# Kernel optimization log

Hardware: AMD Instinct MI355X
Metric: run time of the kernel (lower is better)

## Reference

```python
import jax, jax.numpy as jnp
import numpy as np

BATCH, SEQ_LEN, NOISE_DIM, SEQ_DIM, HID = 8192, 256, 8, 4, 64

def setup_inputs() -> dict:
    key = jax.random.key(0)
    ks = jax.random.split(key, 6)
    s = lambda k, shp, fan: jax.random.normal(k, shp, jnp.float32) * (1.0 / np.sqrt(fan))
    return {
        "noise": jax.random.normal(ks[0], (BATCH, SEQ_LEN, NOISE_DIM), jnp.float32),
        "Wx": s(ks[1], (SEQ_DIM + NOISE_DIM, 4 * HID), SEQ_DIM + NOISE_DIM),
        "Wh": s(ks[2], (HID, 4 * HID), HID),
        "b": jnp.zeros((4 * HID,), jnp.float32),
        "W1": s(ks[3], (HID, HID), HID), "b1": jnp.zeros((HID,), jnp.float32),
        "W2": s(ks[4], (HID, HID), HID), "b2": jnp.zeros((HID,), jnp.float32),
        "W3": s(ks[5], (HID, SEQ_DIM), HID), "b3": jnp.zeros((SEQ_DIM,), jnp.float32),
    }

def reference(noise, Wx, Wh, b, W1, b1, W2, b2, W3, b3):
    batch = noise.shape[0]
    # log_series=True -> initial x is zeros
    x0 = jnp.zeros((batch, SEQ_DIM), noise.dtype)
    h0 = jnp.zeros((batch, HID), noise.dtype)
    c0 = jnp.zeros((batch, HID), noise.dtype)
    noise_t = jnp.swapaxes(noise[:, : SEQ_LEN - 1, :], 0, 1)  # [L-1, B, noise_dim]

    def step(carry, n_t):
        x, h, c = carry
        inp = jnp.concatenate([x, n_t], axis=-1)           # [B, seq_dim+noise_dim]
        z = inp @ Wx + h @ Wh + b                          # [B, 4H], keras gate order i,f,g,o
        i, f, g, o = jnp.split(z, 4, axis=-1)
        c = jax.nn.sigmoid(f) * c + jax.nn.sigmoid(i) * jnp.tanh(g)
        h = jax.nn.sigmoid(o) * jnp.tanh(c)
        y = jax.nn.relu(h @ W1 + b1)
        y = jax.nn.relu(y @ W2 + b2)
        x_new = y @ W3 + b3                                # [B, seq_dim]
        return (x_new, h, c), x_new

    _, xs = jax.lax.scan(step, (x0, h0, c0), noise_t)       # [L-1, B, seq_dim]
    seq = jnp.concatenate([x0[None], xs], axis=0)           # [L, B, seq_dim]
    seq = jnp.swapaxes(seq, 0, 1)                           # [B, L, seq_dim]
    return jnp.cumsum(seq, axis=1)
```

## Files before the change

### kernel.cpp

```cpp
#include <hip/hip_runtime.h>


typedef _Float16 h8 __attribute__((ext_vector_type(8)));
typedef __fp16 p2h __attribute__((ext_vector_type(2)));
typedef float f4 __attribute__((ext_vector_type(4)));

#define MFMA(a, b, c) __builtin_amdgcn_mfma_f32_16x16x32_f16(a, b, c, 0, 0, 0)
#define EXP2(x) __builtin_amdgcn_exp2f(x)

constexpr int SEQ = 256, STEPS = 255, ND = 8, SD = 4, HID = 64, G4 = 256;
constexpr int HST = 72;
constexpr float LOG2E = 1.44269504f;

__device__ __forceinline__ void store4h(_Float16* p, f4 v) {
    p2h lo = __builtin_amdgcn_cvt_pkrtz(v[0], v[1]);
    p2h hi = __builtin_amdgcn_cvt_pkrtz(v[2], v[3]);
    float2 st;
    st.x = __builtin_bit_cast(float, lo);
    st.y = __builtin_bit_cast(float, hi);
    *(float2*)p = st;
}

__global__ __launch_bounds__(256, 2) void genlstm_kernel(
    const float* __restrict__ noise, const float* __restrict__ Wx,
    const float* __restrict__ Wh, const float* __restrict__ b,
    const float* __restrict__ W1, const float* __restrict__ b1,
    const float* __restrict__ W2, const float* __restrict__ b2,
    const float* __restrict__ W3, const float* __restrict__ b3,
    float* __restrict__ out)
{
    __shared__ alignas(16) _Float16 Hb[16 * HST];
    __shared__ alignas(16) _Float16 Y1b[16 * HST];
    __shared__ alignas(16) _Float16 Y2b[16 * HST];

    const int tid = threadIdx.x, wid = tid >> 6, lane = tid & 63;
    const int col = lane & 15, quad = lane >> 4, q8 = quad * 8;
    const int row0 = blockIdx.x * 16;
    const int n0 = wid * 16 + col;
    const int wq = wid * 16 + quad * 4;

    const float gsc[4] = {LOG2E, LOG2E, 2.f * LOG2E, LOG2E};

    h8 wg[4][2];
    #pragma unroll
    for (int g = 0; g < 4; ++g)
        #pragma unroll
        for (int s = 0; s < 2; ++s)
            #pragma unroll
            for (int j = 0; j < 8; ++j)
                wg[g][s][j] = (_Float16)(Wh[(32 * s + q8 + j) * G4 + 64 * g + n0] * gsc[g]);

    h8 wgn[4];
    #pragma unroll
    for (int g = 0; g < 4; ++g)
        #pragma unroll
        for (int j = 0; j < 8; ++j) {
            const int k = q8 + j;
            const int n = 64 * g + n0;
            float v = 0.0f;
            if (k < 8) v = Wx[(4 + k) * G4 + n];
            else if (k == 8) {
                float bx = b3[0] * Wx[0 * G4 + n] + b3[1] * Wx[1 * G4 + n] +
                           b3[2] * Wx[2 * G4 + n] + b3[3] * Wx[3 * G4 + n];
                v = b[n] + bx;
            }
            wgn[g][j] = (_Float16)(v * gsc[g]);
        }

    h8 wgy[4][2];
    #pragma unroll
    for (int s = 0; s < 2; ++s)
        #pragma unroll
        for (int j = 0; j < 8; ++j) {
            const int k = 32 * s + q8 + j;
            const float w30 = W3[k * SD + 0], w31 = W3[k * SD + 1];
            const float w32 = W3[k * SD + 2], w33 = W3[k * SD + 3];
            #pragma unroll
            for (int g = 0; g < 4; ++g) {
                const int n = 64 * g + n0;
                float acc = w30 * Wx[0 * G4 + n] + w31 * Wx[1 * G4 + n] +
                            w32 * Wx[2 * G4 + n] + w33 * Wx[3 * G4 + n];
                wgy[g][s][j] = (_Float16)(acc * gsc[g]);
            }
        }
    h8 w1f[2], w2f[2], w3f[2];
    #pragma unroll
    for (int s = 0; s < 2; ++s)
        #pragma unroll
        for (int j = 0; j < 8; ++j) {
            const int k = 32 * s + q8 + j;
            w1f[s][j] = (_Float16)W1[k * HID + n0];
            w2f[s][j] = (_Float16)W2[k * HID + n0];
            w3f[s][j] = (_Float16)(col < 4 ? W3[k * SD + col] : 0.0f);
        }
    f4 b1v, b2v, b3v;
    #pragma unroll
    for (int r = 0; r < 4; ++r) {
        b1v[r] = b1[wq + r];
        b2v[r] = b2[wq + r];
        b3v[r] = (quad == 0) ? b3[r] : 0.0f;
    }

    if (tid < 16) {
        float4 z; z.x = z.y = z.z = z.w = 0.0f;
        *(float4*)(out + (size_t)(row0 + tid) * SEQ * SD) = z;
    }

    _Float16* Hrow = &Hb[col * HST];
    _Float16* Y1row = &Y1b[col * HST];
    _Float16* Y2row = &Y2b[col * HST];
    float* outp = out + ((size_t)(row0 + col) * SEQ + 1) * SD;

    const float* npt = noise + (size_t)(row0 + col) * SEQ * ND;

    const f4 fz = {0.f, 0.f, 0.f, 0.f};
    f4 cst = fz, run = fz;
    f4 zi, zf, zg, zo;

    float4 nf0, nf1;
    nf0.x = nf0.y = nf0.z = nf0.w = 0.f;
    nf1 = nf0;

    if (blockIdx.x & 256) __builtin_amdgcn_s_sleep(26);

    {
        if (quad == 0) { nf0 = *(const float4*)npt; nf1 = *(const float4*)(npt + 4); }
        npt += ND;
        union { h8 v; p2h p[4]; } nb;
        nb.p[0] = __builtin_amdgcn_cvt_pkrtz(nf0.x, nf0.y);
        nb.p[1] = __builtin_amdgcn_cvt_pkrtz(nf0.z, nf0.w);
        nb.p[2] = __builtin_amdgcn_cvt_pkrtz(nf1.x, nf1.y);
        nb.p[3] = __builtin_amdgcn_cvt_pkrtz(nf1.z, nf1.w);
        #pragma unroll
        for (int g = 0; g < 4; ++g) {
            f4 tb;
            #pragma unroll
            for (int r = 0; r < 4; ++r) tb[r] = b[64 * g + wq + r] * gsc[g];
            f4 z0 = MFMA(wgn[g], nb.v, tb);
            if (g == 0) zi = z0; else if (g == 1) zf = z0;
            else if (g == 2) zg = z0; else zo = z0;
        }
        if (quad == 1) nf0.x = 1.0f;
    }

    #pragma unroll 1
    for (int t = 0; t < STEPS; ++t) {
        if (quad == 0) { nf0 = *(const float4*)npt; nf1 = *(const float4*)(npt + 4); }
        npt += ND;

        f4 hv;
        #pragma unroll
        for (int r = 0; r < 4; ++r) {
            float Ei = EXP2(-fmaxf(zi[r], -15.f * LOG2E));
            float Ef = EXP2(-fmaxf(zf[r], -15.f * LOG2E));
            float Eg = EXP2(-fmaxf(zg[r], -30.f * LOG2E));
            float Eo = EXP2(-zo[r]);
            float Di = 1.f + Ei, Df = 1.f + Ef, Dg = 1.f + Eg, Do = 1.f + Eo;
            float DiDg = Di * Dg;
            float cn = (cst[r] * DiDg + (2.f - Dg) * Df) *
                       __builtin_amdgcn_rcpf(Df * DiDg);
            cst[r] = cn;
            float Ec = EXP2(fmaxf(cn, -15.f) * (-2.f * LOG2E));
            hv[r] = (1.f - Ec) * __builtin_amdgcn_rcpf(Do * (1.f + Ec));
        }
        store4h(Hrow + wq, hv);
        __syncthreads();

        __builtin_amdgcn_s_setprio(1);

        h8 h0 = *(const h8*)(&Hb[col * HST] + q8);
        h8 h1 = *(const h8*)(&Hb[col * HST] + 32 + q8);

        f4 y1 = MFMA(w1f[0], h0, b1v);
        y1 = MFMA(w1f[1], h1, y1);
        #pragma unroll
        for (int r = 0; r < 4; ++r) y1[r] = fmaxf(y1[r], 0.f);
        store4h(Y1row + wq, y1);

        zi = MFMA(wg[0][0], h0, fz); zi = MFMA(wg[0][1], h1, zi);
        zf = MFMA(wg[1][0], h0, fz); zf = MFMA(wg[1][1], h1, zf);
        zg = MFMA(wg[2][0], h0, fz); zg = MFMA(wg[2][1], h1, zg);
        zo = MFMA(wg[3][0], h0, fz); zo = MFMA(wg[3][1], h1, zo);
        __syncthreads();

        h8 p0 = *(const h8*)(Y1row + q8);
        h8 p1 = *(const h8*)(Y1row + 32 + q8);
        f4 y2 = MFMA(w2f[0], p0, b2v);
        y2 = MFMA(w2f[1], p1, y2);
        #pragma unroll
        for (int r = 0; r < 4; ++r) y2[r] = fmaxf(y2[r], 0.f);
        store4h(Y2row + wq, y2);
        __syncthreads();

        h8 q0 = *(const h8*)(Y2row + q8);
        h8 q1 = *(const h8*)(Y2row + 32 + q8);

        zi = MFMA(wgy[0][0], q0, zi); zi = MFMA(wgy[0][1], q1, zi);
        zf = MFMA(wgy[1][0], q0, zf); zf = MFMA(wgy[1][1], q1, zf);
        zg = MFMA(wgy[2][0], q0, zg); zg = MFMA(wgy[2][1], q1, zg);
        zo = MFMA(wgy[3][0], q0, zo); zo = MFMA(wgy[3][1], q1, zo);

        union { h8 v; p2h p[4]; } nb;
        nb.p[0] = __builtin_amdgcn_cvt_pkrtz(nf0.x, nf0.y);
        nb.p[1] = __builtin_amdgcn_cvt_pkrtz(nf0.z, nf0.w);
        nb.p[2] = __builtin_amdgcn_cvt_pkrtz(nf1.x, nf1.y);
        nb.p[3] = __builtin_amdgcn_cvt_pkrtz(nf1.z, nf1.w);
        zi = MFMA(wgn[0], nb.v, zi);
        zf = MFMA(wgn[1], nb.v, zf);
        zg = MFMA(wgn[2], nb.v, zg);
        zo = MFMA(wgn[3], nb.v, zo);

        if (wid == 0) {
            f4 x = MFMA(w3f[0], q0, b3v);
            x = MFMA(w3f[1], q1, x);
            if (quad == 0) {
                run += x;
                *(f4*)outp = run;
            }
        }
        outp += SD;

        __builtin_amdgcn_s_setprio(0);
    }
}

extern "C" void kernel_launch(void* const* d_in, const int* in_sizes, int n_in,
                              void* d_out, int out_size, void* d_ws, size_t ws_size,
                              hipStream_t stream) {
    genlstm_kernel<<<512, 256, 0, stream>>>(
        (const float*)d_in[0], (const float*)d_in[1], (const float*)d_in[2],
        (const float*)d_in[3], (const float*)d_in[4], (const float*)d_in[5],
        (const float*)d_in[6], (const float*)d_in[7], (const float*)d_in[8],
        (const float*)d_in[9], (float*)d_out);
}
```

Baseline: 364.4 us.

## Pair two independent row groups per block with phase-staggered LSTM pipeline

Each block now carries two 16-row groups of four waves each, in 512-thread blocks with half as many blocks. The two groups run the three phases of a step (gate nonlinearity plus output, the Y1 MLP layer, the Y2 layer) offset by one phase, so they share the same barriers. While one group does elementwise and transcendental work, the other issues MFMAs, which is meant to hide the serial dependency chain and barrier latency. The sleep-based stagger is removed. The cost is that each barrier now covers eight waves, and the grid has half as many blocks.

Measured after the change: 623.0 us. 71.0% more time.

```diff
diff --git a/kernel.cpp b/kernel.cpp
--- a/kernel.cpp
+++ b/kernel.cpp
@@ -21,7 +21,7 @@
     *(float2*)p = st;
 }
 
-__global__ __launch_bounds__(256, 2) void genlstm_kernel(
+__global__ __launch_bounds__(512, 2) void genlstm_kernel(
     const float* __restrict__ noise, const float* __restrict__ Wx,
     const float* __restrict__ Wh, const float* __restrict__ b,
     const float* __restrict__ W1, const float* __restrict__ b1,
@@ -29,15 +29,18 @@
     const float* __restrict__ W3, const float* __restrict__ b3,
     float* __restrict__ out)
 {
-    __shared__ alignas(16) _Float16 Hb[16 * HST];
-    __shared__ alignas(16) _Float16 Y1b[16 * HST];
-    __shared__ alignas(16) _Float16 Y2b[16 * HST];
+    __shared__ alignas(16) _Float16 Hb[2][16 * HST];
+    __shared__ alignas(16) _Float16 Y1b[2][16 * HST];
+    __shared__ alignas(16) _Float16 Y2b[2][16 * HST];
 
     const int tid = threadIdx.x, wid = tid >> 6, lane = tid & 63;
+    const int grp = wid >> 2;
+    const int wv = wid & 3;
     const int col = lane & 15, quad = lane >> 4, q8 = quad * 8;
-    const int row0 = blockIdx.x * 16;
-    const int n0 = wid * 16 + col;
-    const int wq = wid * 16 + quad * 4;
+    const int brow = blockIdx.x * 32;
+    const int row0 = brow + grp * 16;
+    const int n0 = wv * 16 + col;
+    const int wq = wv * 16 + quad * 4;
 
     const float gsc[4] = {LOG2E, LOG2E, 2.f * LOG2E, LOG2E};
 
@@ -101,14 +104,14 @@
         b3v[r] = (quad == 0) ? b3[r] : 0.0f;
     }
 
-    if (tid < 16) {
+    if (tid < 32) {
         float4 z; z.x = z.y = z.z = z.w = 0.0f;
-        *(float4*)(out + (size_t)(row0 + tid) * SEQ * SD) = z;
-    }
-
-    _Float16* Hrow = &Hb[col * HST];
-    _Float16* Y1row = &Y1b[col * HST];
-    _Float16* Y2row = &Y2b[col * HST];
+        *(float4*)(out + (size_t)(brow + tid) * SEQ * SD) = z;
+    }
+
+    _Float16* Hrow = &Hb[grp][col * HST];
+    _Float16* Y1row = &Y1b[grp][col * HST];
+    _Float16* Y2row = &Y2b[grp][col * HST];
     float* outp = out + ((size_t)(row0 + col) * SEQ + 1) * SD;
 
     const float* npt = noise + (size_t)(row0 + col) * SEQ * ND;
@@ -120,8 +123,6 @@
     float4 nf0, nf1;
     nf0.x = nf0.y = nf0.z = nf0.w = 0.f;
     nf1 = nf0;
-
-    if (blockIdx.x & 256) __builtin_amdgcn_s_sleep(26);
 
     {
         if (quad == 0) { nf0 = *(const float4*)npt; nf1 = *(const float4*)(npt + 4); }
@@ -143,46 +144,76 @@
         if (quad == 1) nf0.x = 1.0f;
     }
 
-    #pragma unroll 1
-    for (int t = 0; t < STEPS; ++t) {
-        if (quad == 0) { nf0 = *(const float4*)npt; nf1 = *(const float4*)(npt + 4); }
-        npt += ND;
-
-        f4 hv;
-        #pragma unroll
-        for (int r = 0; r < 4; ++r) {
-            float Ei = EXP2(-fmaxf(zi[r], -15.f * LOG2E));
-            float Ef = EXP2(-fmaxf(zf[r], -15.f * LOG2E));
-            float Eg = EXP2(-fmaxf(zg[r], -30.f * LOG2E));
-            float Eo = EXP2(-zo[r]);
-            float Di = 1.f + Ei, Df = 1.f + Ef, Dg = 1.f + Eg, Do = 1.f + Eo;
-            float DiDg = Di * Dg;
-            float cn = (cst[r] * DiDg + (2.f - Dg) * Df) *
-                       __builtin_amdgcn_rcpf(Df * DiDg);
-            cst[r] = cn;
-            float Ec = EXP2(fmaxf(cn, -15.f) * (-2.f * LOG2E));
-            hv[r] = (1.f - Ec) * __builtin_amdgcn_rcpf(Do * (1.f + Ec));
-        }
-        store4h(Hrow + wq, hv);
-        __syncthreads();
-
+    auto segC = [&](int t) {
+        if (t > 0) {
+            h8 q0 = *(const h8*)(Y2row + q8);
+            h8 q1 = *(const h8*)(Y2row + 32 + q8);
+            union { h8 v; p2h p[4]; } nb;
+            nb.p[0] = __builtin_amdgcn_cvt_pkrtz(nf0.x, nf0.y);
+            nb.p[1] = __builtin_amdgcn_cvt_pkrtz(nf0.z, nf0.w);
+            nb.p[2] = __builtin_amdgcn_cvt_pkrtz(nf1.x, nf1.y);
+            nb.p[3] = __builtin_amdgcn_cvt_pkrtz(nf1.z, nf1.w);
+            if (t < STEPS && quad == 0) {
+                nf0 = *(const float4*)npt; nf1 = *(const float4*)(npt + 4);
+            }
+            npt += ND;
+            zi = MFMA(wgn[0], nb.v, zi);
+            zf = MFMA(wgn[1], nb.v, zf);
+            zg = MFMA(wgn[2], nb.v, zg);
+            zo = MFMA(wgn[3], nb.v, zo);
+            zi = MFMA(wgy[0][0], q0, zi); zi = MFMA(wgy[0][1], q1, zi);
+            zf = MFMA(wgy[1][0], q0, zf); zf = MFMA(wgy[1][1], q1, zf);
+            zg = MFMA(wgy[2][0], q0, zg); zg = MFMA(wgy[2][1], q1, zg);
+            zo = MFMA(wgy[3][0], q0, zo); zo = MFMA(wgy[3][1], q1, zo);
+            if (wv == 0) {
+                f4 x = MFMA(w3f[0], q0, b3v);
+                x = MFMA(w3f[1], q1, x);
+                if (quad == 0) {
+                    run += x;
+                    *(f4*)outp = run;
+                }
+            }
+            outp += SD;
+        } else {
+            if (quad == 0) { nf0 = *(const float4*)npt; nf1 = *(const float4*)(npt + 4); }
+            npt += ND;
+        }
+        if (t < STEPS) {
+            f4 hv;
+            #pragma unroll
+            for (int r = 0; r < 4; ++r) {
+                float Ei = EXP2(-fmaxf(zi[r], -15.f * LOG2E));
+                float Ef = EXP2(-fmaxf(zf[r], -15.f * LOG2E));
+                float Eg = EXP2(-fmaxf(zg[r], -30.f * LOG2E));
+                float Eo = EXP2(-zo[r]);
+                float Di = 1.f + Ei, Df = 1.f + Ef, Dg = 1.f + Eg, Do = 1.f + Eo;
+                float DiDg = Di * Dg;
+                float cn = (cst[r] * DiDg + (2.f - Dg) * Df) *
+                           __builtin_amdgcn_rcpf(Df * DiDg);
+                cst[r] = cn;
+                float Ec = EXP2(fmaxf(cn, -15.f) * (-2.f * LOG2E));
+                hv[r] = (1.f - Ec) * __builtin_amdgcn_rcpf(Do * (1.f + Ec));
+            }
+            store4h(Hrow + wq, hv);
+        }
+    };
+    auto segY1 = [&]() {
         __builtin_amdgcn_s_setprio(1);
-
-        h8 h0 = *(const h8*)(&Hb[col * HST] + q8);
-        h8 h1 = *(const h8*)(&Hb[col * HST] + 32 + q8);
-
+        h8 h0 = *(const h8*)(Hrow + q8);
+        h8 h1 = *(const h8*)(Hrow + 32 + q8);
         f4 y1 = MFMA(w1f[0], h0, b1v);
         y1 = MFMA(w1f[1], h1, y1);
         #pragma unroll
         for (int r = 0; r < 4; ++r) y1[r] = fmaxf(y1[r], 0.f);
         store4h(Y1row + wq, y1);
-
         zi = MFMA(wg[0][0], h0, fz); zi = MFMA(wg[0][1], h1, zi);
         zf = MFMA(wg[1][0], h0, fz); zf = MFMA(wg[1][1], h1, zf);
         zg = MFMA(wg[2][0], h0, fz); zg = MFMA(wg[2][1], h1, zg);
         zo = MFMA(wg[3][0], h0, fz); zo = MFMA(wg[3][1], h1, zo);
-        __syncthreads();
-
+        __builtin_amdgcn_s_setprio(0);
+    };
+    auto segY2 = [&]() {
+        __builtin_amdgcn_s_setprio(1);
         h8 p0 = *(const h8*)(Y1row + q8);
         h8 p1 = *(const h8*)(Y1row + 32 + q8);
         f4 y2 = MFMA(w2f[0], p0, b2v);
@@ -190,44 +221,28 @@
         #pragma unroll
         for (int r = 0; r < 4; ++r) y2[r] = fmaxf(y2[r], 0.f);
         store4h(Y2row + wq, y2);
+        __builtin_amdgcn_s_setprio(0);
+    };
+
+    if (grp) segC(0);
+    __syncthreads();
+
+    #pragma unroll 1
+    for (int t = 0; t < STEPS; ++t) {
+        if (!grp) segC(t);   else segY1();
         __syncthreads();
-
-        h8 q0 = *(const h8*)(Y2row + q8);
-        h8 q1 = *(const h8*)(Y2row + 32 + q8);
-
-        zi = MFMA(wgy[0][0], q0, zi); zi = MFMA(wgy[0][1], q1, zi);
-        zf = MFMA(wgy[1][0], q0, zf); zf = MFMA(wgy[1][1], q1, zf);
-        zg = MFMA(wgy[2][0], q0, zg); zg = MFMA(wgy[2][1], q1, zg);
-        zo = MFMA(wgy[3][0], q0, zo); zo = MFMA(wgy[3][1], q1, zo);
-
-        union { h8 v; p2h p[4]; } nb;
-        nb.p[0] = __builtin_amdgcn_cvt_pkrtz(nf0.x, nf0.y);
-        nb.p[1] = __builtin_amdgcn_cvt_pkrtz(nf0.z, nf0.w);
-        nb.p[2] = __builtin_amdgcn_cvt_pkrtz(nf1.x, nf1.y);
-        nb.p[3] = __builtin_amdgcn_cvt_pkrtz(nf1.z, nf1.w);
-        zi = MFMA(wgn[0], nb.v, zi);
-        zf = MFMA(wgn[1], nb.v, zf);
-        zg = MFMA(wgn[2], nb.v, zg);
-        zo = MFMA(wgn[3], nb.v, zo);
-
-        if (wid == 0) {
-            f4 x = MFMA(w3f[0], q0, b3v);
-            x = MFMA(w3f[1], q1, x);
-            if (quad == 0) {
-                run += x;
-                *(f4*)outp = run;
-            }
-        }
-        outp += SD;
-
-        __builtin_amdgcn_s_setprio(0);
-    }
+        if (!grp) segY1();   else segY2();
+        __syncthreads();
+        if (!grp) segY2();   else segC(t + 1);
+        __syncthreads();
+    }
+    if (!grp) segC(STEPS);
 }
 
 extern "C" void kernel_launch(void* const* d_in, const int* in_sizes, int n_in,
                               void* d_out, int out_size, void* d_ws, size_t ws_size,
                               hipStream_t stream) {
-    genlstm_kernel<<<512, 256, 0, stream>>>(
+    genlstm_kernel<<<256, 512, 0, stream>>>(
         (const float*)d_in[0], (const float*)d_in[1], (const float*)d_in[2],
         (const float*)d_in[3], (const float*)d_in[4], (const float*)d_in[5],
         (const float*)d_in[6], (const float*)d_in[7], (const float*)d_in[8],
```

## Split LSTM gate and MLP head work into specialized warp groups

Applied to the files above, without the earlier changes.

Adds two extra wavefronts per block (384 threads) that handle the MLP head (W1, W2, W3 and the output cumsum). The original four waves now compute only the LSTM gates. Barrier counts are matched across both roles: the gate waves issue a double syncthreads while the MLP waves do their two layers. The aim is to take the MLP MFMAs and their register-held weights off the gate waves and ease register pressure, at the cost of more threads per block and the same serial barrier chain.

Result: slower. 608.3 us (+66.9%).

```diff
diff --git a/kernel.cpp b/kernel.cpp
--- a/kernel.cpp
+++ b/kernel.cpp
@@ -21,7 +21,7 @@
     *(float2*)p = st;
 }
 
-__global__ __launch_bounds__(256, 2) void genlstm_kernel(
+__global__ __launch_bounds__(384, 2) void genlstm_kernel(
     const float* __restrict__ noise, const float* __restrict__ Wx,
     const float* __restrict__ Wh, const float* __restrict__ b,
     const float* __restrict__ W1, const float* __restrict__ b1,
@@ -36,198 +36,232 @@
     const int tid = threadIdx.x, wid = tid >> 6, lane = tid & 63;
     const int col = lane & 15, quad = lane >> 4, q8 = quad * 8;
     const int row0 = blockIdx.x * 16;
-    const int n0 = wid * 16 + col;
-    const int wq = wid * 16 + quad * 4;
-
-    const float gsc[4] = {LOG2E, LOG2E, 2.f * LOG2E, LOG2E};
-
-    h8 wg[4][2];
-    #pragma unroll
-    for (int g = 0; g < 4; ++g)
-        #pragma unroll
-        for (int s = 0; s < 2; ++s)
-            #pragma unroll
-            for (int j = 0; j < 8; ++j)
-                wg[g][s][j] = (_Float16)(Wh[(32 * s + q8 + j) * G4 + 64 * g + n0] * gsc[g]);
-
-    h8 wgn[4];
-    #pragma unroll
-    for (int g = 0; g < 4; ++g)
-        #pragma unroll
-        for (int j = 0; j < 8; ++j) {
-            const int k = q8 + j;
-            const int n = 64 * g + n0;
-            float v = 0.0f;
-            if (k < 8) v = Wx[(4 + k) * G4 + n];
-            else if (k == 8) {
-                float bx = b3[0] * Wx[0 * G4 + n] + b3[1] * Wx[1 * G4 + n] +
-                           b3[2] * Wx[2 * G4 + n] + b3[3] * Wx[3 * G4 + n];
-                v = b[n] + bx;
-            }
-            wgn[g][j] = (_Float16)(v * gsc[g]);
-        }
-
-    h8 wgy[4][2];
-    #pragma unroll
-    for (int s = 0; s < 2; ++s)
-        #pragma unroll
-        for (int j = 0; j < 8; ++j) {
-            const int k = 32 * s + q8 + j;
-            const float w30 = W3[k * SD + 0], w31 = W3[k * SD + 1];
-            const float w32 = W3[k * SD + 2], w33 = W3[k * SD + 3];
-            #pragma unroll
-            for (int g = 0; g < 4; ++g) {
-                const int n = 64 * g + n0;
-                float acc = w30 * Wx[0 * G4 + n] + w31 * Wx[1 * G4 + n] +
-                            w32 * Wx[2 * G4 + n] + w33 * Wx[3 * G4 + n];
-                wgy[g][s][j] = (_Float16)(acc * gsc[g]);
-            }
-        }
-    h8 w1f[2], w2f[2], w3f[2];
-    #pragma unroll
-    for (int s = 0; s < 2; ++s)
-        #pragma unroll
-        for (int j = 0; j < 8; ++j) {
-            const int k = 32 * s + q8 + j;
-            w1f[s][j] = (_Float16)W1[k * HID + n0];
-            w2f[s][j] = (_Float16)W2[k * HID + n0];
-            w3f[s][j] = (_Float16)(col < 4 ? W3[k * SD + col] : 0.0f);
-        }
-    f4 b1v, b2v, b3v;
-    #pragma unroll
-    for (int r = 0; r < 4; ++r) {
-        b1v[r] = b1[wq + r];
-        b2v[r] = b2[wq + r];
-        b3v[r] = (quad == 0) ? b3[r] : 0.0f;
-    }
 
     if (tid < 16) {
         float4 z; z.x = z.y = z.z = z.w = 0.0f;
         *(float4*)(out + (size_t)(row0 + tid) * SEQ * SD) = z;
     }
 
-    _Float16* Hrow = &Hb[col * HST];
-    _Float16* Y1row = &Y1b[col * HST];
-    _Float16* Y2row = &Y2b[col * HST];
-    float* outp = out + ((size_t)(row0 + col) * SEQ + 1) * SD;
-
-    const float* npt = noise + (size_t)(row0 + col) * SEQ * ND;
-
-    const f4 fz = {0.f, 0.f, 0.f, 0.f};
-    f4 cst = fz, run = fz;
-    f4 zi, zf, zg, zo;
-
-    float4 nf0, nf1;
-    nf0.x = nf0.y = nf0.z = nf0.w = 0.f;
-    nf1 = nf0;
-
     if (blockIdx.x & 256) __builtin_amdgcn_s_sleep(26);
 
-    {
-        if (quad == 0) { nf0 = *(const float4*)npt; nf1 = *(const float4*)(npt + 4); }
-        npt += ND;
-        union { h8 v; p2h p[4]; } nb;
-        nb.p[0] = __builtin_amdgcn_cvt_pkrtz(nf0.x, nf0.y);
-        nb.p[1] = __builtin_amdgcn_cvt_pkrtz(nf0.z, nf0.w);
-        nb.p[2] = __builtin_amdgcn_cvt_pkrtz(nf1.x, nf1.y);
-        nb.p[3] = __builtin_amdgcn_cvt_pkrtz(nf1.z, nf1.w);
-        #pragma unroll
-        for (int g = 0; g < 4; ++g) {
-            f4 tb;
-            #pragma unroll
-            for (int r = 0; r < 4; ++r) tb[r] = b[64 * g + wq + r] * gsc[g];
-            f4 z0 = MFMA(wgn[g], nb.v, tb);
-            if (g == 0) zi = z0; else if (g == 1) zf = z0;
-            else if (g == 2) zg = z0; else zo = z0;
-        }
-        if (quad == 1) nf0.x = 1.0f;
-    }
-
-    #pragma unroll 1
-    for (int t = 0; t < STEPS; ++t) {
-        if (quad == 0) { nf0 = *(const float4*)npt; nf1 = *(const float4*)(npt + 4); }
-        npt += ND;
-
-        f4 hv;
+    if (wid < 4) {
+        const int wv = wid;
+        const int n0 = wv * 16 + col;
+        const int wq = wv * 16 + quad * 4;
+        const float gsc[4] = {LOG2E, LOG2E, 2.f * LOG2E, LOG2E};
+
+        h8 wg[4][2];
+        #pragma unroll
+        for (int g = 0; g < 4; ++g)
+            #pragma unroll
+            for (int s = 0; s < 2; ++s)
+                #pragma unroll
+                for (int j = 0; j < 8; ++j)
+                    wg[g][s][j] = (_Float16)(Wh[(32 * s + q8 + j) * G4 + 64 * g + n0] * gsc[g]);
+
+        h8 wgn[4];
+        #pragma unroll
+        for (int g = 0; g < 4; ++g)
+            #pragma unroll
+            for (int j = 0; j < 8; ++j) {
+                const int k = q8 + j;
+                const int n = 64 * g + n0;
+                float v = 0.0f;
+                if (k < 8) v = Wx[(4 + k) * G4 + n];
+                else if (k == 8) {
+                    float bx = b3[0] * Wx[0 * G4 + n] + b3[1] * Wx[1 * G4 + n] +
+                               b3[2] * Wx[2 * G4 + n] + b3[3] * Wx[3 * G4 + n];
+                    v = b[n] + bx;
+                }
+                wgn[g][j] = (_Float16)(v * gsc[g]);
+            }
+
+        h8 wgy[4][2];
+        #pragma unroll
+        for (int s = 0; s < 2; ++s)
+            #pragma unroll
+            for (int j = 0; j < 8; ++j) {
+                const int k = 32 * s + q8 + j;
+                const float w30 = W3[k * SD + 0], w31 = W3[k * SD + 1];
+                const float w32 = W3[k * SD + 2], w33 = W3[k * SD + 3];
+                #pragma unroll
+                for (int g = 0; g < 4; ++g) {
+                    const int n = 64 * g + n0;
+                    float acc = w30 * Wx[0 * G4 + n] + w31 * Wx[1 * G4 + n] +
+                                w32 * Wx[2 * G4 + n] + w33 * Wx[3 * G4 + n];
+                    wgy[g][s][j] = (_Float16)(acc * gsc[g]);
+                }
+            }
+
+        _Float16* Hrow = &Hb[col * HST];
+        const _Float16* Y2row = &Y2b[col * HST];
+        const float* npt = noise + (size_t)(row0 + col) * SEQ * ND;
+
+        const f4 fz = {0.f, 0.f, 0.f, 0.f};
+        f4 cst = fz;
+        f4 zi, zf, zg, zo;
+        float4 nf0, nf1;
+        nf0.x = nf0.y = nf0.z = nf0.w = 0.f;
+        nf1 = nf0;
+
+        {
+            if (quad == 0) { nf0 = *(const float4*)npt; nf1 = *(const float4*)(npt + 4); }
+            npt += ND;
+            union { h8 v; p2h p[4]; } nb;
+            nb.p[0] = __builtin_amdgcn_cvt_pkrtz(nf0.x, nf0.y);
+            nb.p[1] = __builtin_amdgcn_cvt_pkrtz(nf0.z, nf0.w);
+            nb.p[2] = __builtin_amdgcn_cvt_pkrtz(nf1.x, nf1.y);
+            nb.p[3] = __builtin_amdgcn_cvt_pkrtz(nf1.z, nf1.w);
+            #pragma unroll
+            for (int g = 0; g < 4; ++g) {
+                f4 tb;
+                #pragma unroll
+                for (int r = 0; r < 4; ++r) tb[r] = b[64 * g + wq + r] * gsc[g];
+                f4 z0 = MFMA(wgn[g], nb.v, tb);
+                if (g == 0) zi = z0; else if (g == 1) zf = z0;
+                else if (g == 2) zg = z0; else zo = z0;
+            }
+            if (quad == 1) nf0.x = 1.0f;
+        }
+
+        __builtin_amdgcn_s_setprio(1);
+        #pragma unroll 1
+        for (int t = 0; t < STEPS; ++t) {
+            if (quad == 0) { nf0 = *(const float4*)npt; nf1 = *(const float4*)(npt + 4); }
+            npt += ND;
+
+            f4 hv;
+            #pragma unroll
+            for (int r = 0; r < 4; ++r) {
+                float Ei = EXP2(-fmaxf(zi[r], -15.f * LOG2E));
+                float Ef = EXP2(-fmaxf(zf[r], -15.f * LOG2E));
+                float Eg = EXP2(-fmaxf(zg[r], -30.f * LOG2E));
+                float Eo = EXP2(-zo[r]);
+                float Di = 1.f + Ei, Df = 1.f + Ef, Dg = 1.f + Eg, Do = 1.f + Eo;
+                float DiDg = Di * Dg;
+                float cn = (cst[r] * DiDg + (2.f - Dg) * Df) *
+                           __builtin_amdgcn_rcpf(Df * DiDg);
+                cst[r] = cn;
+                float Ec = EXP2(fmaxf(cn, -15.f) * (-2.f * LOG2E));
+                hv[r] = (1.f - Ec) * __builtin_amdgcn_rcpf(Do * (1.f + Ec));
+            }
+            store4h(Hrow + wq, hv);
+            __syncthreads();
+            __builtin_amdgcn_s_setprio(0);
+
+            zi = MFMA(wg[0][0], *(const h8*)(Hrow + q8), fz);
+            zi = MFMA(wg[0][1], *(const h8*)(Hrow + 32 + q8), zi);
+            {
+                h8 h0 = *(const h8*)(Hrow + q8);
+                h8 h1 = *(const h8*)(Hrow + 32 + q8);
+                zf = MFMA(wg[1][0], h0, fz); zf = MFMA(wg[1][1], h1, zf);
+                zg = MFMA(wg[2][0], h0, fz); zg = MFMA(wg[2][1], h1, zg);
+                zo = MFMA(wg[3][0], h0, fz); zo = MFMA(wg[3][1], h1, zo);
+            }
+            __syncthreads();
+            __syncthreads();
+            __builtin_amdgcn_s_setprio(1);
+
+            h8 q0 = *(const h8*)(Y2row + q8);
+            h8 q1 = *(const h8*)(Y2row + 32 + q8);
+            union { h8 v; p2h p[4]; } nb;
+            nb.p[0] = __builtin_amdgcn_cvt_pkrtz(nf0.x, nf0.y);
+            nb.p[1] = __builtin_amdgcn_cvt_pkrtz(nf0.z, nf0.w);
+            nb.p[2] = __builtin_amdgcn_cvt_pkrtz(nf1.x, nf1.y);
+            nb.p[3] = __builtin_amdgcn_cvt_pkrtz(nf1.z, nf1.w);
+            zi = MFMA(wgn[0], nb.v, zi);
+            zf = MFMA(wgn[1], nb.v, zf);
+            zg = MFMA(wgn[2], nb.v, zg);
+            zo = MFMA(wgn[3], nb.v, zo);
+            zi = MFMA(wgy[0][0], q0, zi); zi = MFMA(wgy[0][1], q1, zi);
+            zf = MFMA(wgy[1][0], q0, zf); zf = MFMA(wgy[1][1], q1, zf);
+            zg = MFMA(wgy[2][0], q0, zg); zg = MFMA(wgy[2][1], q1, zg);
+            zo = MFMA(wgy[3][0], q0, zo); zo = MFMA(wgy[3][1], q1, zo);
+        }
+    } else {
+        const int mw = wid - 4;
+        h8 w1m[2][2], w2m[2][2], w3f[2];
+        #pragma unroll
+        for (int tn = 0; tn < 2; ++tn)
+            #pragma unroll
+            for (int s = 0; s < 2; ++s)
+                #pragma unroll
+                for (int j = 0; j < 8; ++j) {
+                    const int k = 32 * s + q8 + j;
+                    const int n = 32 * mw + 16 * tn + col;
+                    w1m[tn][s][j] = (_Float16)W1[k * HID + n];
+                    w2m[tn][s][j] = (_Float16)W2[k * HID + n];
+                }
+        #pragma unroll
+        for (int s = 0; s < 2; ++s)
+            #pragma unroll
+            for (int j = 0; j < 8; ++j) {
+                const int k = 32 * s + q8 + j;
+                w3f[s][j] = (_Float16)((mw == 0 && col < 4) ? W3[k * SD + col] : 0.0f);
+            }
+        f4 b1m[2], b2m[2], b3v;
         #pragma unroll
         for (int r = 0; r < 4; ++r) {
-            float Ei = EXP2(-fmaxf(zi[r], -15.f * LOG2E));
-            float Ef = EXP2(-fmaxf(zf[r], -15.f * LOG2E));
-            float Eg = EXP2(-fmaxf(zg[r], -30.f * LOG2E));
-            float Eo = EXP2(-zo[r]);
-            float Di = 1.f + Ei, Df = 1.f + Ef, Dg = 1.f + Eg, Do = 1.f + Eo;
-            float DiDg = Di * Dg;
-            float cn = (cst[r] * DiDg + (2.f - Dg) * Df) *
-                       __builtin_amdgcn_rcpf(Df * DiDg);
-            cst[r] = cn;
-            float Ec = EXP2(fmaxf(cn, -15.f) * (-2.f * LOG2E));
-            hv[r] = (1.f - Ec) * __builtin_amdgcn_rcpf(Do * (1.f + Ec));
-        }
-        store4h(Hrow + wq, hv);
-        __syncthreads();
+            #pragma unroll
+            for (int tn = 0; tn < 2; ++tn) {
+                b1m[tn][r] = b1[32 * mw + 16 * tn + quad * 4 + r];
+                b2m[tn][r] = b2[32 * mw + 16 * tn + quad * 4 + r];
+            }
+            b3v[r] = (quad == 0) ? b3[r] : 0.0f;
+        }
+
+        const _Float16* Hrow = &Hb[col * HST];
+        _Float16* Y1row = &Y1b[col * HST];
+        _Float16* Y2row = &Y2b[col * HST];
+        float* outp = out + ((size_t)(row0 + col) * SEQ + 1) * SD;
+        const f4 fz = {0.f, 0.f, 0.f, 0.f};
+        f4 run = fz;
 
         __builtin_amdgcn_s_setprio(1);
-
-        h8 h0 = *(const h8*)(&Hb[col * HST] + q8);
-        h8 h1 = *(const h8*)(&Hb[col * HST] + 32 + q8);
-
-        f4 y1 = MFMA(w1f[0], h0, b1v);
-        y1 = MFMA(w1f[1], h1, y1);
-        #pragma unroll
-        for (int r = 0; r < 4; ++r) y1[r] = fmaxf(y1[r], 0.f);
-        store4h(Y1row + wq, y1);
-
-        zi = MFMA(wg[0][0], h0, fz); zi = MFMA(wg[0][1], h1, zi);
-        zf = MFMA(wg[1][0], h0, fz); zf = MFMA(wg[1][1], h1, zf);
-        zg = MFMA(wg[2][0], h0, fz); zg = MFMA(wg[2][1], h1, zg);
-        zo = MFMA(wg[3][0], h0, fz); zo = MFMA(wg[3][1], h1, zo);
-        __syncthreads();
-
-        h8 p0 = *(const h8*)(Y1row + q8);
-        h8 p1 = *(const h8*)(Y1row + 32 + q8);
-        f4 y2 = MFMA(w2f[0], p0, b2v);
-        y2 = MFMA(w2f[1], p1, y2);
-        #pragma unroll
-        for (int r = 0; r < 4; ++r) y2[r] = fmaxf(y2[r], 0.f);
-        store4h(Y2row + wq, y2);
-        __syncthreads();
-
-        h8 q0 = *(const h8*)(Y2row + q8);
-        h8 q1 = *(const h8*)(Y2row + 32 + q8);
-
-        zi = MFMA(wgy[0][0], q0, zi); zi = MFMA(wgy[0][1], q1, zi);
-        zf = MFMA(wgy[1][0], q0, zf); zf = MFMA(wgy[1][1], q1, zf);
-        zg = MFMA(wgy[2][0], q0, zg); zg = MFMA(wgy[2][1], q1, zg);
-        zo = MFMA(wgy[3][0], q0, zo); zo = MFMA(wgy[3][1], q1, zo);
-
-        union { h8 v; p2h p[4]; } nb;
-        nb.p[0] = __builtin_amdgcn_cvt_pkrtz(nf0.x, nf0.y);
-        nb.p[1] = __builtin_amdgcn_cvt_pkrtz(nf0.z, nf0.w);
-        nb.p[2] = __builtin_amdgcn_cvt_pkrtz(nf1.x, nf1.y);
-        nb.p[3] = __builtin_amdgcn_cvt_pkrtz(nf1.z, nf1.w);
-        zi = MFMA(wgn[0], nb.v, zi);
-        zf = MFMA(wgn[1], nb.v, zf);
-        zg = MFMA(wgn[2], nb.v, zg);
-        zo = MFMA(wgn[3], nb.v, zo);
-
-        if (wid == 0) {
-            f4 x = MFMA(w3f[0], q0, b3v);
-            x = MFMA(w3f[1], q1, x);
-            if (quad == 0) {
-                run += x;
-                *(f4*)outp = run;
-            }
-        }
-        outp += SD;
-
-        __builtin_amdgcn_s_setprio(0);
+        #pragma unroll 1
+        for (int t = 0; t < STEPS; ++t) {
+            __syncthreads();
+            h8 h0 = *(const h8*)(Hrow + q8);
+            h8 h1 = *(const h8*)(Hrow + 32 + q8);
+            #pragma unroll
+            for (int tn = 0; tn < 2; ++tn) {
+                f4 y1 = MFMA(w1m[tn][0], h0, b1m[tn]);
+                y1 = MFMA(w1m[tn][1], h1, y1);
+                #pragma unroll
+                for (int r = 0; r < 4; ++r) y1[r] = fmaxf(y1[r], 0.f);
+                store4h(Y1row + 32 * mw + 16 * tn + 4 * quad, y1);
+            }
+            __syncthreads();
+            h8 p0 = *(const h8*)(Y1row + q8);
+            h8 p1 = *(const h8*)(Y1row + 32 + q8);
+            #pragma unroll
+            for (int tn = 0; tn < 2; ++tn) {
+                f4 y2 = MFMA(w2m[tn][0], p0, b2m[tn]);
+                y2 = MFMA(w2m[tn][1], p1, y2);
+                #pragma unroll
+                for (int r = 0; r < 4; ++r) y2[r] = fmaxf(y2[r], 0.f);
+                store4h(Y2row + 32 * mw + 16 * tn + 4 * quad, y2);
+            }
+            __syncthreads();
+            if (mw == 0) {
+                h8 q0 = *(const h8*)(Y2row + q8);
+                h8 q1 = *(const h8*)(Y2row + 32 + q8);
+                f4 x = MFMA(w3f[0], q0, b3v);
+                x = MFMA(w3f[1], q1, x);
+                if (quad == 0) {
+                    run += x;
+                    *(f4*)outp = run;
+                }
+            }
+            outp += SD;
+        }
     }
 }
 
 extern "C" void kernel_launch(void* const* d_in, const int* in_sizes, int n_in,
                               void* d_out, int out_size, void* d_ws, size_t ws_size,
                               hipStream_t stream) {
-    genlstm_kernel<<<512, 256, 0, stream>>>(
+    genlstm_kernel<<<512, 384, 0, stream>>>(
         (const float*)d_in[0], (const float*)d_in[1], (const float*)d_in[2],
         (const float*)d_in[3], (const float*)d_in[4], (const float*)d_in[5],
         (const float*)d_in[6], (const float*)d_in[7], (const float*)d_in[8],
```
